# Kernel tuning notes

Hardware: AMD Instinct MI355X
Metric: run time of the kernel (lower is better)

## Reference

```python
import jax, jax.numpy as jnp
import numpy as np

BS, T, FIN, FOUT = 8, 1024, 512, 512
ALPHA = 0.1      # leaky relu slope
T_K = 3          # t_ksize (odd); temporal band radius = T_K // 2
S_K = 4          # s_ksize semantic topk
NEG_INF = -9e15


def setup_inputs() -> dict:
    key = jax.random.key(0)
    k1, k2, k3, k4 = jax.random.split(key, 4)
    # xavier-uniform-ish scales (gain 1.414)
    w_lim = 1.414 * np.sqrt(6.0 / (FIN + FOUT))
    a_lim = 1.414 * np.sqrt(6.0 / (2 * FOUT + 1))
    return {
        "x_a": jax.random.normal(k1, (BS, T, FIN), jnp.float32),
        "x_v": jax.random.normal(k2, (BS, T, FIN), jnp.float32),
        "W": jax.random.uniform(k3, (FIN, FOUT), jnp.float32, -w_lim, w_lim),
        "a": jax.random.uniform(k4, (2 * FOUT, 1), jnp.float32, -a_lim, a_lim),
    }


def _temporal_mask(t):
    # tem_adj[i,j] = 1 iff |i-j| <= T_K//2 and i, j on the same side of t-0.5
    idx = jnp.arange(2 * t)
    same_side = (idx[:, None] >= t) == (idx[None, :] >= t)
    band = jnp.abs(idx[:, None] - idx[None, :]) <= (T_K // 2)
    return band & same_side  # (2t, 2t) bool


def _semantic_block_mask(x, k):
    # x: (bs, t, d). Top-k neighbors by negative squared euclidean distance.
    inner = 2.0 * jnp.einsum("btd,bsd->bts", x, x)
    sq = jnp.sum(x * x, axis=-1, keepdims=True)  # (bs, t, 1)
    pd = -(sq - inner + jnp.swapaxes(sq, -1, -2))  # (bs, t, t)
    _, idx = jax.lax.top_k(pd, k)  # (bs, t, k)
    bs, t = x.shape[0], x.shape[1]
    b_ix = jnp.arange(bs)[:, None, None]
    r_ix = jnp.arange(t)[None, :, None]
    return jnp.zeros((bs, t, t), bool).at[b_ix, r_ix, idx].set(True)


def reference(x_a, x_v, W, a):
    bs, t, _ = x_a.shape
    h = jnp.concatenate([x_a, x_v], axis=1)          # (bs, 2t, FIN)
    Wh = h @ W                                        # (bs, 2t, FOUT)

    # additive GAT score: e = leakyrelu(Wh a1 + (Wh a2)^T)
    Wh1 = Wh @ a[:FOUT]                               # (bs, 2t, 1)
    Wh2 = Wh @ a[FOUT:]                               # (bs, 2t, 1)
    e = Wh1 + jnp.swapaxes(Wh2, -1, -2)               # (bs, 2t, 2t)
    e = jnp.where(e > 0, e, ALPHA * e)                # leaky relu

    # adjacency: temporal band + semantic topk within aa / vv blocks
    tem = _temporal_mask(t)                           # (2t, 2t)
    sem_aa = _semantic_block_mask(Wh[:, :t], S_K)     # (bs, t, t)
    sem_vv = _semantic_block_mask(Wh[:, t:], S_K)     # (bs, t, t)
    zb = jnp.zeros((bs, t, t), bool)
    sem = jnp.concatenate([
        jnp.concatenate([sem_aa, zb], axis=-1),
        jnp.concatenate([zb, sem_vv], axis=-1),
    ], axis=1)                                        # (bs, 2t, 2t)
    mask = tem[None] | sem

    attention = jax.nn.softmax(jnp.where(mask, e, NEG_INF), axis=-1)
    h_prime = jax.nn.elu(attention @ Wh)              # (bs, 2t, FOUT)
    return h_prime[:, :t], h_prime[:, t:]
```

## Files before the change

kernel.cpp:

```cpp
#include <hip/hip_runtime.h>
#include <math.h>

#define T_ 1024
#define BS_ 8
#define D_ 512
#define NROWS_ (BS_*2*T_)
#define ALPHA_ 0.1f

typedef _Float16 f16;
typedef _Float16 f16x8 __attribute__((ext_vector_type(8)));
typedef _Float16 f16x4 __attribute__((ext_vector_type(4)));
typedef _Float16 f16x2 __attribute__((ext_vector_type(2)));
typedef float f32x4 __attribute__((ext_vector_type(4)));

#define MFMA16(A,B,C) __builtin_amdgcn_mfma_f32_16x16x32_f16((A),(B),(C),0,0,0)

__device__ __forceinline__ void gl16(const void* g, void* l) {
    __builtin_amdgcn_global_load_lds(
        (const __attribute__((address_space(1))) unsigned int*)g,
        (__attribute__((address_space(3))) unsigned int*)l, 16, 0, 0);
}

#if __has_builtin(__builtin_amdgcn_fdot2)
__device__ __forceinline__ float fdot2p(f16x2 a, f16x2 b, float c) {
    return __builtin_amdgcn_fdot2(a, b, c, false);
}
#else
__device__ __forceinline__ float fdot2p(f16x2 a, f16x2 b, float c) {
    return fmaf((float)a[1], (float)b[1], fmaf((float)a[0], (float)b[0], c));
}
#endif

__device__ __forceinline__ float fdot8(const f16x8 a, const f16x8 b, float s) {
    #pragma unroll
    for (int q = 0; q < 4; ++q) {
        f16x2 aa, bb;
        aa[0] = a[2*q]; aa[1] = a[2*q+1];
        bb[0] = b[2*q]; bb[1] = b[2*q+1];
        s = fdot2p(aa, bb, s);
    }
    return s;
}

__device__ __forceinline__ unsigned sortable(float f) {
    unsigned u = __float_as_uint(f);
    return u ^ ((u & 0x80000000u) ? 0xFFFFFFFFu : 0x80000000u);
}
__device__ __forceinline__ unsigned pack_key(float s, int col) {
    return (sortable(s) & 0xFFFFFC00u) | (unsigned)(1023 - col);
}

#define INSK4(K, X) { \
    bool g3 = (X) > K[3], g2 = (X) > K[2], g1 = (X) > K[1], g0 = (X) > K[0]; \
    K[3] = g2 ? K[2] : (g3 ? (X) : K[3]); \
    K[2] = g1 ? K[1] : (g2 ? (X) : K[2]); \
    K[1] = g0 ? K[0] : (g1 ? (X) : K[1]); \
    K[0] = g0 ? (X) : K[0]; }

#define INSK8(K, X) { \
    bool h7=(X)>K[7],h6=(X)>K[6],h5=(X)>K[5],h4=(X)>K[4]; \
    bool h3=(X)>K[3],h2=(X)>K[2],h1=(X)>K[1],h0=(X)>K[0]; \
    K[7]=h6?K[6]:(h7?(X):K[7]); K[6]=h5?K[5]:(h6?(X):K[6]); \
    K[5]=h4?K[4]:(h5?(X):K[5]); K[4]=h3?K[3]:(h4?(X):K[4]); \
    K[3]=h2?K[2]:(h3?(X):K[3]); K[2]=h1?K[1]:(h2?(X):K[2]); \
    K[1]=h0?K[0]:(h1?(X):K[1]); K[0]=h0?(X):K[0]; }

#define CEU(a,b) { unsigned mx_ = (a) > (b) ? (a) : (b); \
    unsigned mn_ = (a) > (b) ? (b) : (a); (a) = mx_; (b) = mn_; }

#define MERGE8(K, MSK) { \
    unsigned b0=__shfl_xor(K[0],MSK), b1=__shfl_xor(K[1],MSK), \
             b2=__shfl_xor(K[2],MSK), b3=__shfl_xor(K[3],MSK), \
             b4=__shfl_xor(K[4],MSK), b5=__shfl_xor(K[5],MSK), \
             b6=__shfl_xor(K[6],MSK), b7=__shfl_xor(K[7],MSK); \
    K[0]=K[0]>b7?K[0]:b7; K[1]=K[1]>b6?K[1]:b6; \
    K[2]=K[2]>b5?K[2]:b5; K[3]=K[3]>b4?K[3]:b4; \
    K[4]=K[4]>b3?K[4]:b3; K[5]=K[5]>b2?K[5]:b2; \
    K[6]=K[6]>b1?K[6]:b1; K[7]=K[7]>b0?K[7]:b0; \
    CEU(K[0],K[4]); CEU(K[1],K[5]); CEU(K[2],K[6]); CEU(K[3],K[7]); \
    CEU(K[0],K[2]); CEU(K[1],K[3]); CEU(K[4],K[6]); CEU(K[5],K[7]); \
    CEU(K[0],K[1]); CEU(K[2],K[3]); CEU(K[4],K[5]); CEU(K[6],K[7]); }

#define BETTER(x,xi,v,vi) ((x) > (v) || ((x) == (v) && (xi) < (vi)))
#define INS4T(TV,TI,X,ID) { \
    bool g3 = BETTER(X,ID,TV[3],TI[3]), g2 = BETTER(X,ID,TV[2],TI[2]); \
    bool g1 = BETTER(X,ID,TV[1],TI[1]), g0 = BETTER(X,ID,TV[0],TI[0]); \
    TV[3] = g2 ? TV[2] : (g3 ? (X) : TV[3]); TI[3] = g2 ? TI[2] : (g3 ? (ID) : TI[3]); \
    TV[2] = g1 ? TV[1] : (g2 ? (X) : TV[2]); TI[2] = g1 ? TI[1] : (g2 ? (ID) : TI[2]); \
    TV[1] = g0 ? TV[0] : (g1 ? (X) : TV[1]); TI[1] = g0 ? TI[0] : (g1 ? (ID) : TI[1]); \
    TV[0] = g0 ? (X) : TV[0]; TI[0] = g0 ? (ID) : TI[0]; }

#define PIPE_WAIT5() { asm volatile("s_waitcnt vmcnt(5)" ::: "memory"); \
    __builtin_amdgcn_s_barrier(); __builtin_amdgcn_sched_barrier(0); }
#define PIPE_WAIT0() { asm volatile("s_waitcnt vmcnt(0)" ::: "memory"); \
    __builtin_amdgcn_s_barrier(); __builtin_amdgcn_sched_barrier(0); }

__global__ __launch_bounds__(256) void k_splitW(
    const float* __restrict__ W, f16* __restrict__ WTh, f16* __restrict__ WTl)
{
    __shared__ float tile[64][65];
    const int tid = threadIdx.x;
    const int tk = (blockIdx.x >> 3) << 6, tn = (blockIdx.x & 7) << 6;
    const int r0 = tid >> 4, c4 = (tid & 15) << 2;

    #pragma unroll
    for (int rr = 0; rr < 4; ++rr) {
        int k = r0 + (rr << 4);
        float4 v = *(const float4*)(W + (size_t)(tk + k) * D_ + tn + c4);
        tile[k][c4+0] = v.x; tile[k][c4+1] = v.y;
        tile[k][c4+2] = v.z; tile[k][c4+3] = v.w;
    }
    __syncthreads();
    #pragma unroll
    for (int rr = 0; rr < 4; ++rr) {
        int n = r0 + (rr << 4);
        f16x4 h, l;
        #pragma unroll
        for (int i = 0; i < 4; ++i) {
            float x = tile[c4 + i][n];
            f16 hh = (f16)x; h[i] = hh; l[i] = (f16)(x - (float)hh);
        }
        *(f16x4*)(WTh + (size_t)(tn + n) * D_ + tk + c4) = h;
        *(f16x4*)(WTl + (size_t)(tn + n) * D_ + tk + c4) = l;
    }
}

__global__ __launch_bounds__(512, 2) void k_gemm_wh(
    const float* __restrict__ xa, const float* __restrict__ xv,
    const f16* __restrict__ WTh, const f16* __restrict__ WTl,
    const float* __restrict__ a,
    f16* __restrict__ Whh, f16* __restrict__ Whl,
    float* __restrict__ Wh1, float* __restrict__ Wh2, float* __restrict__ sq)
{
    __shared__ __align__(16) unsigned char smem[122880];

    const int tid  = threadIdx.x;
    const int w    = tid >> 6;
    const int wr   = w >> 2, wc = w & 3;
    const int lane = tid & 63;
    const int l15  = lane & 15;
    const int g    = lane >> 4;
    const int bid  = blockIdx.x;
    const int swz  = ((bid & 7) << 5) + (bid >> 3);
    const int rowbase = swz << 6;

    const int qp = rowbase >> 10;
    const float* xsrc = ((qp & 1) ? xv : xa)
                      + (size_t)((qp >> 1) * 1024 + (rowbase & 1023)) * D_;
    const char* xsrcB = (const char*)xsrc;
    const char* WThB = (const char*)WTh;
    const char* WTlB = (const char*)WTl;

    const int rB1 = tid >> 2,          cB1 = tid & 3;
    const int jB1 = cB1 ^ ((rB1 >> 1) & 3);
    const int rB2 = (tid + 512) >> 2,  cB2 = tid & 3;
    const int jB2 = cB2 ^ ((rB2 >> 1) & 3);

    const int rA = tid >> 3, cA = tid & 7;
    const int jcA = (((cA >> 1) ^ ((rA >> 1) & 3)) << 1) | (cA & 1);
    const size_t gaA_base = (size_t)rA * 2048 + (jcA << 4);

    const int swzx = (g ^ ((l15 >> 1) & 3)) << 4;
    const int bo0 = (((wc << 6) +  0 + l15) << 6) + swzx;
    const int bo1 = (((wc << 6) + 16 + l15) << 6) + swzx;
    const int bo2 = (((wc << 6) + 32 + l15) << 6) + swzx;
    const int bo3 = (((wc << 6) + 48 + l15) << 6) + swzx;
    const int arow = (wr << 5) + l15;
    const int ar0 = (arow << 7) + ((g ^ ((arow >> 1) & 3)) << 5);

    #define STAGE(kc_, cq_, bb_) { \
        const size_t g1_ = ((size_t)(((cq_) << 8) + rB1) << 10) + ((size_t)(kc_) << 6) + (jB1 << 4); \
        const size_t g2_ = ((size_t)(((cq_) << 8) + rB2) << 10) + ((size_t)(kc_) << 6) + (jB2 << 4); \
        gl16(WThB + g1_, smem + (bb_) + (tid << 4)); \
        gl16(WThB + g2_, smem + (bb_) + ((tid + 512) << 4)); \
        gl16(WTlB + g1_, smem + (bb_) + 16384 + (tid << 4)); \
        gl16(WTlB + g2_, smem + (bb_) + 16384 + ((tid + 512) << 4)); \
        gl16(xsrcB + gaA_base + ((size_t)(kc_) << 7), smem + (bb_) + 32768 + (tid << 4)); }

    #define CONVA(H, L, p0, p1) { \
        float xs_[8] = {p0[0],p0[1],p0[2],p0[3],p1[0],p1[1],p1[2],p1[3]}; \
        _Pragma("unroll") \
        for (int e_ = 0; e_ < 8; ++e_) { \
            f16 hh_ = (f16)xs_[e_]; H[e_] = hh_; L[e_] = (f16)(xs_[e_] - (float)hh_); } }

    #define COMPUTE(ACC, BB) { \
        f32x4 u0 = *(const f32x4*)(smem + (BB) + 32768 + ar0); \
        f32x4 u1 = *(const f32x4*)(smem + (BB) + 32768 + ar0 + 16); \
        f32x4 v0 = *(const f32x4*)(smem + (BB) + 32768 + ar0 + 2048); \
        f32x4 v1 = *(const f32x4*)(smem + (BB) + 32768 + ar0 + 2048 + 16); \
        f16x8 AH0, AL0, AH1, AL1; \
        CONVA(AH0, AL0, u0, u1); \
        CONVA(AH1, AL1, v0, v1); \
        f16x8 bh0 = *(const f16x8*)(smem + (BB) + bo0); \
        f16x8 bh1 = *(const f16x8*)(smem + (BB) + bo1); \
        f16x8 bh2 = *(const f16x8*)(smem + (BB) + bo2); \
        f16x8 bh3 = *(const f16x8*)(smem + (BB) + bo3); \
        f16x8 bl0 = *(const f16x8*)(smem + (BB) + 16384 + bo0); \
        f16x8 bl1 = *(const f16x8*)(smem + (BB) + 16384 + bo1); \
        f16x8 bl2 = *(const f16x8*)(smem + (BB) + 16384 + bo2); \
        f16x8 bl3 = *(const f16x8*)(smem + (BB) + 16384 + bo3); \
        ACC[0][0] = MFMA16(AH0, bh0, ACC[0][0]); \
        ACC[0][1] = MFMA16(AH0, bh1, ACC[0][1]); \
        ACC[0][2] = MFMA16(AH0, bh2, ACC[0][2]); \
        ACC[0][3] = MFMA16(AH0, bh3, ACC[0][3]); \
        ACC[1][0] = MFMA16(AH1, bh0, ACC[1][0]); \
        ACC[1][1] = MFMA16(AH1, bh1, ACC[1][1]); \
        ACC[1][2] = MFMA16(AH1, bh2, ACC[1][2]); \
        ACC[1][3] = MFMA16(AH1, bh3, ACC[1][3]); \
        ACC[0][0] = MFMA16(AL0, bh0, ACC[0][0]); \
        ACC[0][1] = MFMA16(AL0, bh1, ACC[0][1]); \
        ACC[0][2] = MFMA16(AL0, bh2, ACC[0][2]); \
        ACC[0][3] = MFMA16(AL0, bh3, ACC[0][3]); \
        ACC[1][0] = MFMA16(AL1, bh0, ACC[1][0]); \
        ACC[1][1] = MFMA16(AL1, bh1, ACC[1][1]); \
        ACC[1][2] = MFMA16(AL1, bh2, ACC[1][2]); \
        ACC[1][3] = MFMA16(AL1, bh3, ACC[1][3]); \
        ACC[0][0] = MFMA16(AH0, bl0, ACC[0][0]); \
        ACC[0][1] = MFMA16(AH0, bl1, ACC[0][1]); \
        ACC[0][2] = MFMA16(AH0, bl2, ACC[0][2]); \
        ACC[0][3] = MFMA16(AH0, bl3, ACC[0][3]); \
        ACC[1][0] = MFMA16(AH1, bl0, ACC[1][0]); \
        ACC[1][1] = MFMA16(AH1, bl1, ACC[1][1]); \
        ACC[1][2] = MFMA16(AH1, bl2, ACC[1][2]); \
        ACC[1][3] = MFMA16(AH1, bl3, ACC[1][3]); }

    f32x4 acc0[2][4], acc1[2][4];
    #pragma unroll
    for (int m = 0; m < 2; ++m)
        #pragma unroll
        for (int c = 0; c < 4; ++c) {
            acc0[m][c] = (f32x4){0.f,0.f,0.f,0.f};
            acc1[m][c] = (f32x4){0.f,0.f,0.f,0.f};
        }

    STAGE(0, 0, 0);
    STAGE(0, 1, 40960);

    int cb = 0;
    int sb = 81920;
    for (int t = 0; t < 31; ++t) {
        PIPE_WAIT5();
        if (t <= 29) {
            const int tau = t + 2;
            STAGE(tau >> 1, tau & 1, sb);
        }
        if (!(t & 1)) { COMPUTE(acc0, cb); }
        else          { COMPUTE(acc1, cb); }
        cb += 40960; cb = (cb == 122880) ? 0 : cb;
        sb += 40960; sb = (sb == 122880) ? 0 : sb;
    }
    PIPE_WAIT0();
    COMPUTE(acc1, cb);
    #undef STAGE
    #undef COMPUTE
    #undef CONVA

    __syncthreads();

    float st1[8], st2[8], stq[8];
    #pragma unroll
    for (int s = 0; s < 8; ++s) { st1[s] = 0.f; st2[s] = 0.f; stq[s] = 0.f; }

    #define EPI(ACC, CQ) { \
        _Pragma("unroll") \
        for (int c = 0; c < 4; ++c) { \
            const int col = ((CQ) << 8) + (wc << 6) + (c << 4) + l15; \
            const float a1 = a[col]; \
            const float a2 = a[512 + col]; \
            _Pragma("unroll") \
            for (int m = 0; m < 2; ++m) \
            _Pragma("unroll") \
            for (int j = 0; j < 4; ++j) { \
                const float v = ACC[m][c][j]; \
                const int slot = (m << 2) + j; \
                st1[slot] = fmaf(v, a1, st1[slot]); \
                st2[slot] = fmaf(v, a2, st2[slot]); \
                stq[slot] = fmaf(v, v,  stq[slot]); \
                f16 h = (f16)v; f16 l = (f16)(v - (float)h); \
                const size_t off = (size_t)(rowbase + (wr << 5) + (m << 4) + (g << 2) + j) * D_ + col; \
                Whh[off] = h; Whl[off] = l; \
            } } }

    EPI(acc0, 0);
    EPI(acc1, 1);
    #undef EPI

    #pragma unroll
    for (int mask = 1; mask < 16; mask <<= 1)
        #pragma unroll
        for (int s = 0; s < 8; ++s) {
            st1[s] += __shfl_xor(st1[s], mask);
            st2[s] += __shfl_xor(st2[s], mask);
            stq[s] += __shfl_xor(stq[s], mask);
        }
    if (l15 == 0) {
        #pragma unroll
        for (int s = 0; s < 8; ++s) {
            const int rl = (wr << 5) + ((s >> 2) << 4) + (g << 2) + (s & 3);
            float* sp = (float*)smem + ((rl << 2) + wc) * 3;
            sp[0] = st1[s]; sp[1] = st2[s]; sp[2] = stq[s];
        }
    }
    __syncthreads();
    if (tid < 64) {
        float s1 = 0.f, s2 = 0.f, s3 = 0.f;
        #pragma unroll
        for (int wv = 0; wv < 4; ++wv) {
            const float* sp = (const float*)smem + ((tid << 2) + wv) * 3;
            s1 += sp[0]; s2 += sp[1]; s3 += sp[2];
        }
        Wh1[rowbase + tid] = s1; Wh2[rowbase + tid] = s2; sq[rowbase + tid] = s3;
    }
}

__global__ __launch_bounds__(512, 1) void k_gram_topk8(
    const f16* __restrict__ Whh, const float* __restrict__ sq,
    int* __restrict__ topk8)
{
    __shared__ __align__(16) unsigned char smem[81920];

    const int bid = blockIdx.x;
    const int swz = ((bid & 7) << 5) + (bid >> 3);
    const int p   = swz >> 4;
    const int rt  = swz & 15;
    const int rowbase  = (p << 10) + (rt << 6);
    const int colPanel = p << 10;

    const int tid  = threadIdx.x;
    const int w    = tid >> 6;
    const int wr   = w >> 2, wc = w & 3;
    const int lane = tid & 63;
    const int l15  = lane & 15;
    const int g    = lane >> 4;
    const int r8   = lane >> 3;
    const int k7   = lane & 7;
    const int sw2  = ((k7 ^ r8) << 4);
    const int q0x  = ((g ^ (lane & 7)) << 4);

    const int rowA = tid >> 3;
    const int k7A  = tid & 7;
    const int aswz = ((k7A ^ (rowA & 7)) << 4);

    const char* WB = (const char*)Whh;

    const int aoff0 = 32768 + (((wr << 5) +  0 + l15) << 7) + q0x;
    const int aoff1 = 32768 + (((wr << 5) + 16 + l15) << 7) + q0x;
    const int boff0 = (((wc << 6) +  0 + l15) << 7) + q0x;
    const int boff1 = (((wc << 6) + 16 + l15) << 7) + q0x;
    const int boff2 = (((wc << 6) + 32 + l15) << 7) + q0x;
    const int boff3 = (((wc << 6) + 48 + l15) << 7) + q0x;

    f32x4 acc[2][4];
    #pragma unroll
    for (int m = 0; m < 2; ++m)
        #pragma unroll
        for (int c = 0; c < 4; ++c) acc[m][c] = (f32x4){0.f,0.f,0.f,0.f};

    unsigned k4[8][4];
    #pragma unroll
    for (int s = 0; s < 8; ++s)
        #pragma unroll
        for (int q = 0; q < 4; ++q) k4[s][q] = 0u;

    #define STAGE_G(t) { \
        const int ct_ = (t) >> 3, kc_ = (t) & 7; \
        const int bufb_ = ((t) & 1) * 40960; \
        size_t gB_ = ((size_t)(colPanel + (ct_ << 8) + (w << 5) + r8) << 10) + (kc_ << 7) + sw2; \
        int ldsB_ = bufb_ + (w << 12) + (lane << 4); \
        _Pragma("unroll") \
        for (int j_ = 0; j_ < 4; ++j_) { \
            gl16(WB + gB_, smem + ldsB_); \
            gB_ += (size_t)8 << 10; ldsB_ += 1024; \
        } \
        size_t gA_ = ((size_t)(rowbase + rowA) << 10) + (kc_ << 7) + aswz; \
        gl16(WB + gA_, smem + bufb_ + 32768 + (tid << 4)); \
    }

    STAGE_G(0);

    for (int t = 0; t < 32; ++t) {
        __syncthreads();
        if (t < 31) STAGE_G(t + 1);
        const int bufb = (t & 1) * 40960;

        #pragma unroll
        for (int s = 0; s < 2; ++s) {
            const int sx = s << 6;
            f16x8 a0 = *(const f16x8*)(smem + bufb + (aoff0 ^ sx));
            f16x8 a1 = *(const f16x8*)(smem + bufb + (aoff1 ^ sx));
            f16x8 b0 = *(const f16x8*)(smem + bufb + (boff0 ^ sx));
            f16x8 b1 = *(const f16x8*)(smem + bufb + (boff1 ^ sx));
            f16x8 b2 = *(const f16x8*)(smem + bufb + (boff2 ^ sx));
            f16x8 b3 = *(const f16x8*)(smem + bufb + (boff3 ^ sx));
            acc[0][0] = MFMA16(a0, b0, acc[0][0]);
            acc[0][1] = MFMA16(a0, b1, acc[0][1]);
            acc[0][2] = MFMA16(a0, b2, acc[0][2]);
            acc[0][3] = MFMA16(a0, b3, acc[0][3]);
            acc[1][0] = MFMA16(a1, b0, acc[1][0]);
            acc[1][1] = MFMA16(a1, b1, acc[1][1]);
            acc[1][2] = MFMA16(a1, b2, acc[1][2]);
            acc[1][3] = MFMA16(a1, b3, acc[1][3]);
        }

        if ((t & 7) == 7) {
            const int ct = t >> 3;
            #pragma unroll
            for (int c = 0; c < 4; ++c) {
                const int cl = (ct << 8) + (wc << 6) + (c << 4) + l15;
                const float sqc = sq[colPanel + cl];
                #pragma unroll
                for (int m = 0; m < 2; ++m)
                    #pragma unroll
                    for (int j = 0; j < 4; ++j) {
                        float sc = fmaf(2.f, acc[m][c][j], -sqc);
                        unsigned key = pack_key(sc, cl);
                        INSK4(k4[(m << 2) + j], key);
                    }
                acc[0][c] = (f32x4){0.f,0.f,0.f,0.f};
                acc[1][c] = (f32x4){0.f,0.f,0.f,0.f};
            }
        }
    }

    unsigned k8[8][8];
    #pragma unroll
    for (int s = 0; s < 8; ++s) {
        #pragma unroll
        for (int q = 0; q < 4; ++q) { k8[s][q] = k4[s][q]; k8[s][4 + q] = 0u; }
    }
    #pragma unroll
    for (int msk = 1; msk < 16; msk <<= 1) {
        #pragma unroll
        for (int s = 0; s < 8; ++s) { MERGE8(k8[s], msk); }
    }

    if (l15 == 0) {
        #pragma unroll
        for (int s = 0; s < 8; ++s) {
            const int row_local = ((s >> 2) << 4) + (g << 2) + (s & 3);
            const int off = ((((wr << 5) + row_local) << 2) + wc) << 5;
            *(uint4*)(smem + off)      = make_uint4(k8[s][0], k8[s][1], k8[s][2], k8[s][3]);
            *(uint4*)(smem + off + 16) = make_uint4(k8[s][4], k8[s][5], k8[s][6], k8[s][7]);
        }
    }
    __syncthreads();
    if (tid < 64) {
        const unsigned* bp = (const unsigned*)smem + (tid << 5);
        unsigned kk[8];
        #pragma unroll
        for (int s = 0; s < 8; ++s) kk[s] = bp[s];
        #pragma unroll
        for (int wv = 1; wv < 4; ++wv)
            #pragma unroll
            for (int s = 0; s < 8; ++s) { unsigned x = bp[(wv << 3) + s]; INSK8(kk, x); }
        #pragma unroll
        for (int s = 0; s < 8; ++s)
            topk8[(((size_t)(rowbase + tid)) << 3) + s] = 1023 - (int)(kk[s] & 1023u);
    }
    #undef STAGE_G
}

__global__ __launch_bounds__(256) void k_rescore_agg(
    const f16* __restrict__ Whh, const f16* __restrict__ Whl,
    const float* __restrict__ Wh1, const float* __restrict__ Wh2,
    const float* __restrict__ sq, const int* __restrict__ topk8,
    float* __restrict__ out)
{
    const int bid = blockIdx.x;
    const int swz = ((bid & 7) << 9) + (bid >> 3);
    const int tid  = threadIdx.x;
    const int lane = tid & 63;
    const int r    = (swz << 2) + (tid >> 6);
    const int p    = r >> 10;
    const int i    = r & 1023;
    const int rb   = p << 10;

    const size_t ro = (size_t)r * D_ + (lane << 3);
    f16x8 ah = *(const f16x8*)(Whh + ro);
    f16x8 al = *(const f16x8*)(Whl + ro);

    int cid[8];
    {
        int4 t0 = *(const int4*)(topk8 + ((size_t)r << 3));
        int4 t1 = *(const int4*)(topk8 + ((size_t)r << 3) + 4);
        cid[0]=t0.x; cid[1]=t0.y; cid[2]=t0.z; cid[3]=t0.w;
        cid[4]=t1.x; cid[5]=t1.y; cid[6]=t1.z; cid[7]=t1.w;
    }

    float dp[8];
    #pragma unroll
    for (int c = 0; c < 8; ++c) {
        const size_t co = (size_t)(rb + cid[c]) * D_ + (lane << 3);
        f16x8 bh = *(const f16x8*)(Whh + co);
        f16x8 bl = *(const f16x8*)(Whl + co);
        float s = 0.f;
        s = fdot8(ah, bh, s);
        s = fdot8(ah, bl, s);
        s = fdot8(al, bh, s);
        dp[c] = s;
    }
    #pragma unroll
    for (int off = 32; off > 0; off >>= 1)
        #pragma unroll
        for (int c = 0; c < 8; ++c) dp[c] += __shfl_xor(dp[c], off);

    float tv[4] = {-3.4e38f,-3.4e38f,-3.4e38f,-3.4e38f};
    int   ti[4] = {0x7FFFFFFF,0x7FFFFFFF,0x7FFFFFFF,0x7FFFFFFF};
    #pragma unroll
    for (int c = 0; c < 8; ++c) {
        float sc = fmaf(2.f, dp[c], -sq[rb + cid[c]]);
        INS4T(tv, ti, sc, cid[c]);
    }

    const int  tM = i - 1, tC = i, tP = i + 1;
    const bool vM = (i > 0), vP = (i < T_ - 1);
    const int s0 = ti[0], s1 = ti[1], s2 = ti[2], s3 = ti[3];

    bool u0 = !((vM && s0 == tM) || (s0 == tC) || (vP && s0 == tP));
    bool u1 = !((vM && s1 == tM) || (s1 == tC) || (vP && s1 == tP));
    bool u2 = !((vM && s2 == tM) || (s2 == tC) || (vP && s2 == tP));
    bool u3 = !((vM && s3 == tM) || (s3 == tC) || (vP && s3 == tP));

    int  ci[7] = { vM ? tM : 0, tC, vP ? tP : 0, s0, s1, s2, s3 };
    bool cv[7] = { vM, true, vP, u0, u1, u2, u3 };

    f16x8 vhq[7];
    #pragma unroll
    for (int q = 0; q < 7; ++q)
        vhq[q] = *(const f16x8*)(Whh + (size_t)(rb + ci[q]) * D_ + (lane << 3));

    const float e1 = Wh1[r];
    float ev[7];
    float m = -3.4e38f;
    #pragma unroll
    for (int q = 0; q < 7; ++q) {
        float e = e1 + Wh2[rb + ci[q]];
        e = (e > 0.f) ? e : ALPHA_ * e;
        e = cv[q] ? e : -3.4e38f;
        ev[q] = e;
        m = fmaxf(m, e);
    }
    float wsum = 0.f;
    #pragma unroll
    for (int q = 0; q < 7; ++q) {
        float wq = cv[q] ? expf(ev[q] - m) : 0.f;
        ev[q] = wq;
        wsum += wq;
    }
    #pragma unroll
    for (int q = 0; q < 7; ++q) ev[q] /= wsum;

    float A[8] = {0.f,0.f,0.f,0.f,0.f,0.f,0.f,0.f};
    #pragma unroll
    for (int q = 0; q < 7; ++q) {
        const float wq = ev[q];
        #pragma unroll
        for (int e = 0; e < 8; ++e) A[e] = fmaf(wq, (float)vhq[q][e], A[e]);
    }
    #pragma unroll
    for (int e = 0; e < 8; ++e)
        A[e] = (A[e] > 0.f) ? A[e] : expm1f(A[e]);

    const int blk = p & 1, b = p >> 1;
    float* dst = out + (size_t)blk * ((size_t)BS_ * T_ * D_)
               + ((size_t)((b << 10) + i)) * D_ + (lane << 3);
    *(float4*)(dst)     = make_float4(A[0], A[1], A[2], A[3]);
    *(float4*)(dst + 4) = make_float4(A[4], A[5], A[6], A[7]);
}

extern "C" void kernel_launch(void* const* d_in, const int* in_sizes, int n_in,
                              void* d_out, int out_size, void* d_ws, size_t ws_size,
                              hipStream_t stream)
{
    const float* xa = (const float*)d_in[0];
    const float* xv = (const float*)d_in[1];
    const float* W  = (const float*)d_in[2];
    const float* a  = (const float*)d_in[3];
    float* out = (float*)d_out;

    f16* Whh    = (f16*)d_ws;
    f16* Whl    = Whh + (size_t)NROWS_ * D_;
    f16* WTh    = Whl + (size_t)NROWS_ * D_;
    f16* WTl    = WTh + (size_t)D_ * D_;
    float* Wh1  = (float*)(WTl + (size_t)D_ * D_);
    float* Wh2  = Wh1 + NROWS_;
    float* sq   = Wh2 + NROWS_;
    int* topk8  = (int*)(sq + NROWS_);

    k_splitW     <<<dim3(64),   dim3(256), 0, stream>>>(W, WTh, WTl);
    k_gemm_wh    <<<dim3(256),  dim3(512), 0, stream>>>(xa, xv, WTh, WTl, a, Whh, Whl, Wh1, Wh2, sq);
    k_gram_topk8 <<<dim3(256),  dim3(512), 0, stream>>>(Whh, sq, topk8);
    k_rescore_agg<<<dim3(4096), dim3(256), 0, stream>>>(Whh, Whl, Wh1, Wh2, sq, topk8, out);
}
```

Before: 119.4 us.

## Shrink Wh GEMM B-stage tiles to raise occupancy and coalesce epilogue stores via LDS

Result: slower. 138.1 us (+15.7%).

```diff
diff --git a/kernel.cpp b/kernel.cpp
--- a/kernel.cpp
+++ b/kernel.cpp
@@ -90,7 +90,7 @@
     TV[1] = g0 ? TV[0] : (g1 ? (X) : TV[1]); TI[1] = g0 ? TI[0] : (g1 ? (ID) : TI[1]); \
     TV[0] = g0 ? (X) : TV[0]; TI[0] = g0 ? (ID) : TI[0]; }
 
-#define PIPE_WAIT5() { asm volatile("s_waitcnt vmcnt(5)" ::: "memory"); \
+#define PIPE_WAIT3() { asm volatile("s_waitcnt vmcnt(3)" ::: "memory"); \
     __builtin_amdgcn_s_barrier(); __builtin_amdgcn_sched_barrier(0); }
 #define PIPE_WAIT0() { asm volatile("s_waitcnt vmcnt(0)" ::: "memory"); \
     __builtin_amdgcn_s_barrier(); __builtin_amdgcn_sched_barrier(0); }
@@ -125,14 +125,14 @@
     }
 }
 
-__global__ __launch_bounds__(512, 2) void k_gemm_wh(
+__global__ __launch_bounds__(512, 4) void k_gemm_wh(
     const float* __restrict__ xa, const float* __restrict__ xv,
     const f16* __restrict__ WTh, const f16* __restrict__ WTl,
     const float* __restrict__ a,
     f16* __restrict__ Whh, f16* __restrict__ Whl,
     float* __restrict__ Wh1, float* __restrict__ Wh2, float* __restrict__ sq)
 {
-    __shared__ __align__(16) unsigned char smem[122880];
+    __shared__ __align__(16) unsigned char smem[73728];
 
     const int tid  = threadIdx.x;
     const int w    = tid >> 6;
@@ -151,31 +151,24 @@
     const char* WThB = (const char*)WTh;
     const char* WTlB = (const char*)WTl;
 
-    const int rB1 = tid >> 2,          cB1 = tid & 3;
-    const int jB1 = cB1 ^ ((rB1 >> 1) & 3);
-    const int rB2 = (tid + 512) >> 2,  cB2 = tid & 3;
-    const int jB2 = cB2 ^ ((rB2 >> 1) & 3);
-
+    const int rB = tid >> 2, cB = tid & 3;
+    const int jB = cB ^ ((rB >> 1) & 3);
     const int rA = tid >> 3, cA = tid & 7;
     const int jcA = (((cA >> 1) ^ ((rA >> 1) & 3)) << 1) | (cA & 1);
     const size_t gaA_base = (size_t)rA * 2048 + (jcA << 4);
 
-    const int swzx = (g ^ ((l15 >> 1) & 3)) << 4;
-    const int bo0 = (((wc << 6) +  0 + l15) << 6) + swzx;
-    const int bo1 = (((wc << 6) + 16 + l15) << 6) + swzx;
-    const int bo2 = (((wc << 6) + 32 + l15) << 6) + swzx;
-    const int bo3 = (((wc << 6) + 48 + l15) << 6) + swzx;
+    const int swzB = (g ^ ((l15 >> 1) & 3)) << 4;
+    const int bo0 = (((wc << 5) + l15) << 6) + swzB;
+    const int bo1 = bo0 + 1024;
     const int arow = (wr << 5) + l15;
-    const int ar0 = (arow << 7) + ((g ^ ((arow >> 1) & 3)) << 5);
-
-    #define STAGE(kc_, cq_, bb_) { \
-        const size_t g1_ = ((size_t)(((cq_) << 8) + rB1) << 10) + ((size_t)(kc_) << 6) + (jB1 << 4); \
-        const size_t g2_ = ((size_t)(((cq_) << 8) + rB2) << 10) + ((size_t)(kc_) << 6) + (jB2 << 4); \
-        gl16(WThB + g1_, smem + (bb_) + (tid << 4)); \
-        gl16(WThB + g2_, smem + (bb_) + ((tid + 512) << 4)); \
-        gl16(WTlB + g1_, smem + (bb_) + 16384 + (tid << 4)); \
-        gl16(WTlB + g2_, smem + (bb_) + 16384 + ((tid + 512) << 4)); \
-        gl16(xsrcB + gaA_base + ((size_t)(kc_) << 7), smem + (bb_) + 32768 + (tid << 4)); }
+    const int ar0 = 16384 + (arow << 7) + ((g ^ ((l15 >> 1) & 3)) << 5);
+
+    #define STAGE(tau_, bb_) { \
+        const int kc_ = (tau_) >> 2, cq_ = (tau_) & 3; \
+        const size_t gB_ = ((size_t)((cq_ << 7) + rB) << 10) + ((size_t)kc_ << 6) + (jB << 4); \
+        gl16(WThB + gB_, smem + (bb_) + (tid << 4)); \
+        gl16(WTlB + gB_, smem + (bb_) + 8192 + (tid << 4)); \
+        gl16(xsrcB + gaA_base + ((size_t)kc_ << 7), smem + (bb_) + 16384 + (tid << 4)); }
 
     #define CONVA(H, L, p0, p1) { \
         float xs_[8] = {p0[0],p0[1],p0[2],p0[3],p1[0],p1[1],p1[2],p1[3]}; \
@@ -184,73 +177,64 @@
             f16 hh_ = (f16)xs_[e_]; H[e_] = hh_; L[e_] = (f16)(xs_[e_] - (float)hh_); } }
 
     #define COMPUTE(ACC, BB) { \
-        f32x4 u0 = *(const f32x4*)(smem + (BB) + 32768 + ar0); \
-        f32x4 u1 = *(const f32x4*)(smem + (BB) + 32768 + ar0 + 16); \
-        f32x4 v0 = *(const f32x4*)(smem + (BB) + 32768 + ar0 + 2048); \
-        f32x4 v1 = *(const f32x4*)(smem + (BB) + 32768 + ar0 + 2048 + 16); \
+        f32x4 u0 = *(const f32x4*)(smem + (BB) + ar0); \
+        f32x4 u1 = *(const f32x4*)(smem + (BB) + ar0 + 16); \
+        f32x4 v0 = *(const f32x4*)(smem + (BB) + ar0 + 2048); \
+        f32x4 v1 = *(const f32x4*)(smem + (BB) + ar0 + 2048 + 16); \
         f16x8 AH0, AL0, AH1, AL1; \
         CONVA(AH0, AL0, u0, u1); \
         CONVA(AH1, AL1, v0, v1); \
         f16x8 bh0 = *(const f16x8*)(smem + (BB) + bo0); \
         f16x8 bh1 = *(const f16x8*)(smem + (BB) + bo1); \
-        f16x8 bh2 = *(const f16x8*)(smem + (BB) + bo2); \
-        f16x8 bh3 = *(const f16x8*)(smem + (BB) + bo3); \
-        f16x8 bl0 = *(const f16x8*)(smem + (BB) + 16384 + bo0); \
-        f16x8 bl1 = *(const f16x8*)(smem + (BB) + 16384 + bo1); \
-        f16x8 bl2 = *(const f16x8*)(smem + (BB) + 16384 + bo2); \
-        f16x8 bl3 = *(const f16x8*)(smem + (BB) + 16384 + bo3); \
+        f16x8 bl0 = *(const f16x8*)(smem + (BB) + 8192 + bo0); \
+        f16x8 bl1 = *(const f16x8*)(smem + (BB) + 8192 + bo1); \
         ACC[0][0] = MFMA16(AH0, bh0, ACC[0][0]); \
         ACC[0][1] = MFMA16(AH0, bh1, ACC[0][1]); \
-        ACC[0][2] = MFMA16(AH0, bh2, ACC[0][2]); \
-        ACC[0][3] = MFMA16(AH0, bh3, ACC[0][3]); \
         ACC[1][0] = MFMA16(AH1, bh0, ACC[1][0]); \
         ACC[1][1] = MFMA16(AH1, bh1, ACC[1][1]); \
-        ACC[1][2] = MFMA16(AH1, bh2, ACC[1][2]); \
-        ACC[1][3] = MFMA16(AH1, bh3, ACC[1][3]); \
         ACC[0][0] = MFMA16(AL0, bh0, ACC[0][0]); \
         ACC[0][1] = MFMA16(AL0, bh1, ACC[0][1]); \
-        ACC[0][2] = MFMA16(AL0, bh2, ACC[0][2]); \
-        ACC[0][3] = MFMA16(AL0, bh3, ACC[0][3]); \
         ACC[1][0] = MFMA16(AL1, bh0, ACC[1][0]); \
         ACC[1][1] = MFMA16(AL1, bh1, ACC[1][1]); \
-        ACC[1][2] = MFMA16(AL1, bh2, ACC[1][2]); \
-        ACC[1][3] = MFMA16(AL1, bh3, ACC[1][3]); \
         ACC[0][0] = MFMA16(AH0, bl0, ACC[0][0]); \
         ACC[0][1] = MFMA16(AH0, bl1, ACC[0][1]); \
-        ACC[0][2] = MFMA16(AH0, bl2, ACC[0][2]); \
-        ACC[0][3] = MFMA16(AH0, bl3, ACC[0][3]); \
         ACC[1][0] = MFMA16(AH1, bl0, ACC[1][0]); \
-        ACC[1][1] = MFMA16(AH1, bl1, ACC[1][1]); \
-        ACC[1][2] = MFMA16(AH1, bl2, ACC[1][2]); \
-        ACC[1][3] = MFMA16(AH1, bl3, ACC[1][3]); }
-
-    f32x4 acc0[2][4], acc1[2][4];
+        ACC[1][1] = MFMA16(AH1, bl1, ACC[1][1]); }
+
+    f32x4 accA[2][2], accB[2][2], accC[2][2], accD[2][2];
     #pragma unroll
     for (int m = 0; m < 2; ++m)
         #pragma unroll
-        for (int c = 0; c < 4; ++c) {
-            acc0[m][c] = (f32x4){0.f,0.f,0.f,0.f};
-            acc1[m][c] = (f32x4){0.f,0.f,0.f,0.f};
-        }
-
-    STAGE(0, 0, 0);
-    STAGE(0, 1, 40960);
-
-    int cb = 0;
-    int sb = 81920;
-    for (int t = 0; t < 31; ++t) {
-        PIPE_WAIT5();
-        if (t <= 29) {
-            const int tau = t + 2;
-            STAGE(tau >> 1, tau & 1, sb);
-        }
-        if (!(t & 1)) { COMPUTE(acc0, cb); }
-        else          { COMPUTE(acc1, cb); }
-        cb += 40960; cb = (cb == 122880) ? 0 : cb;
-        sb += 40960; sb = (sb == 122880) ? 0 : sb;
-    }
+        for (int c = 0; c < 2; ++c) {
+            accA[m][c] = (f32x4){0.f,0.f,0.f,0.f};
+            accB[m][c] = (f32x4){0.f,0.f,0.f,0.f};
+            accC[m][c] = (f32x4){0.f,0.f,0.f,0.f};
+            accD[m][c] = (f32x4){0.f,0.f,0.f,0.f};
+        }
+
+    STAGE(0, 0);
+    STAGE(1, 24576);
+
+    int tau = 2;
+    int sb  = 49152;
+    int cb  = 0;
+    #define ADV(p_) { p_ += 24576; if (p_ == 73728) p_ = 0; }
+    #define STEPX(ACC) { \
+        PIPE_WAIT3(); \
+        STAGE(tau, sb); ++tau; ADV(sb); \
+        COMPUTE(ACC, cb); ADV(cb); }
+
+    for (int kk = 0; kk < 15; ++kk) {
+        STEPX(accA); STEPX(accB); STEPX(accC); STEPX(accD);
+    }
+    STEPX(accA);
+    STEPX(accB);
+    PIPE_WAIT3();
+    COMPUTE(accC, cb); ADV(cb);
     PIPE_WAIT0();
-    COMPUTE(acc1, cb);
+    COMPUTE(accD, cb);
+    #undef STEPX
+    #undef ADV
     #undef STAGE
     #undef COMPUTE
     #undef CONVA
@@ -261,10 +245,12 @@
     #pragma unroll
     for (int s = 0; s < 8; ++s) { st1[s] = 0.f; st2[s] = 0.f; stq[s] = 0.f; }
 
-    #define EPI(ACC, CQ) { \
+    f16* dump = (f16*)smem;
+
+    #define DUMP_HI(ACC, CQ) { \
         _Pragma("unroll") \
-        for (int c = 0; c < 4; ++c) { \
-            const int col = ((CQ) << 8) + (wc << 6) + (c << 4) + l15; \
+        for (int c = 0; c < 2; ++c) { \
+            const int col = ((CQ) << 7) + (wc << 5) + (c << 4) + l15; \
             const float a1 = a[col]; \
             const float a2 = a[512 + col]; \
             _Pragma("unroll") \
@@ -276,14 +262,46 @@
                 st1[slot] = fmaf(v, a1, st1[slot]); \
                 st2[slot] = fmaf(v, a2, st2[slot]); \
                 stq[slot] = fmaf(v, v,  stq[slot]); \
-                f16 h = (f16)v; f16 l = (f16)(v - (float)h); \
-                const size_t off = (size_t)(rowbase + (wr << 5) + (m << 4) + (g << 2) + j) * D_ + col; \
-                Whh[off] = h; Whl[off] = l; \
+                const int row = (wr << 5) + (m << 4) + (g << 2) + j; \
+                dump[(row << 9) + col] = (f16)v; \
             } } }
 
-    EPI(acc0, 0);
-    EPI(acc1, 1);
-    #undef EPI
+    #define DUMP_LO(ACC, CQ) { \
+        _Pragma("unroll") \
+        for (int c = 0; c < 2; ++c) { \
+            const int col = ((CQ) << 7) + (wc << 5) + (c << 4) + l15; \
+            _Pragma("unroll") \
+            for (int m = 0; m < 2; ++m) \
+            _Pragma("unroll") \
+            for (int j = 0; j < 4; ++j) { \
+                const float v = ACC[m][c][j]; \
+                const f16 h = (f16)v; \
+                const int row = (wr << 5) + (m << 4) + (g << 2) + j; \
+                dump[(row << 9) + col] = (f16)(v - (float)h); \
+            } } }
+
+    DUMP_HI(accA, 0); DUMP_HI(accB, 1); DUMP_HI(accC, 2); DUMP_HI(accD, 3);
+    __syncthreads();
+    {
+        const f16* srcp = dump + (tid << 6);
+        f16* dstp = Whh + ((size_t)rowbase << 9) + (tid << 6);
+        #pragma unroll
+        for (int k = 0; k < 8; ++k)
+            *(f16x8*)(dstp + (k << 3)) = *(const f16x8*)(srcp + (k << 3));
+    }
+    __syncthreads();
+    DUMP_LO(accA, 0); DUMP_LO(accB, 1); DUMP_LO(accC, 2); DUMP_LO(accD, 3);
+    __syncthreads();
+    {
+        const f16* srcp = dump + (tid << 6);
+        f16* dstp = Whl + ((size_t)rowbase << 9) + (tid << 6);
+        #pragma unroll
+        for (int k = 0; k < 8; ++k)
+            *(f16x8*)(dstp + (k << 3)) = *(const f16x8*)(srcp + (k << 3));
+    }
+    __syncthreads();
+    #undef DUMP_HI
+    #undef DUMP_LO
 
     #pragma unroll
     for (int mask = 1; mask < 16; mask <<= 1)
@@ -297,7 +315,7 @@
         #pragma unroll
         for (int s = 0; s < 8; ++s) {
             const int rl = (wr << 5) + ((s >> 2) << 4) + (g << 2) + (s & 3);
-            float* sp = (float*)smem + ((rl << 2) + wc) * 3;
+            float* sp = (float*)(smem + 65536) + ((rl << 2) + wc) * 3;
             sp[0] = st1[s]; sp[1] = st2[s]; sp[2] = stq[s];
         }
     }
@@ -306,7 +324,7 @@
         float s1 = 0.f, s2 = 0.f, s3 = 0.f;
         #pragma unroll
         for (int wv = 0; wv < 4; ++wv) {
-            const float* sp = (const float*)smem + ((tid << 2) + wv) * 3;
+            const float* sp = (const float*)(smem + 65536) + ((tid << 2) + wv) * 3;
             s1 += sp[0]; s2 += sp[1]; s3 += sp[2];
         }
         Wh1[rowbase + tid] = s1; Wh2[rowbase + tid] = s2; sq[rowbase + tid] = s3;
```
